# Kernel optimization log

Measured on AMD Instinct MI355X. Metric: run time of the kernel, lower is better.

The kernel has to match this reference:

```python
import jax, jax.numpy as jnp
import numpy as np

B, S, D = 2, 2048, 1024
H, DQK, DV = 16, 64, 64

def setup_inputs() -> dict:
    key = jax.random.key(0)
    k1, k2, k3, k4, k5 = jax.random.split(key, 5)
    scale_in = 1.0 / np.sqrt(D)
    scale_v = 1.0 / np.sqrt(H * DV)
    return {
        "x":   jax.random.normal(k1, (B, S, D), dtype=jnp.float32),
        "W_q": jax.random.uniform(k2, (D, H * DQK), minval=-scale_in, maxval=scale_in, dtype=jnp.float32),
        "W_k": jax.random.uniform(k3, (D, H * DQK), minval=-scale_in, maxval=scale_in, dtype=jnp.float32),
        "W_v": jax.random.uniform(k4, (D, H * DV), minval=-scale_in, maxval=scale_in, dtype=jnp.float32),
        "W_o": jax.random.uniform(k5, (H * DV, D), minval=-scale_v, maxval=scale_v, dtype=jnp.float32),
    }

def reference(x, W_q, W_k, W_v, W_o):
    b, s, _ = x.shape
    # projections -> [B, H, S, d]
    Q = (x @ W_q).reshape(b, s, H, DQK).transpose(0, 2, 1, 3)
    K = (x @ W_k).reshape(b, s, H, DQK).transpose(0, 2, 1, 3)
    V = (x @ W_v).reshape(b, s, H, DV).transpose(0, 2, 1, 3)
    scores = jnp.einsum('bhqd,bhkd->bhqk', Q, K) / np.sqrt(DQK).astype(np.float32)
    causal_mask = jnp.triu(jnp.ones((s, s), dtype=bool), k=1)  # True above diagonal
    scores = jnp.where(causal_mask[None, None], -jnp.inf, scores)
    attn = jax.nn.softmax(scores, axis=-1)
    out = jnp.einsum('bhqk,bhkd->bhqd', attn, V)  # [B,H,S,DV]
    out = out.transpose(0, 2, 1, 3).reshape(b, s, H * DV)
    return out @ W_o
```

## Files before the change

kernel.cpp:

```cpp
#include <hip/hip_runtime.h>


typedef float  f32x4  __attribute__((ext_vector_type(4)));
typedef __bf16 bf16x8 __attribute__((ext_vector_type(8)));

__device__ __forceinline__ unsigned short f2bf(float f) {
    __bf16 h = (__bf16)f;
    return __builtin_bit_cast(unsigned short, h);
}

__device__ __forceinline__ void gld16(unsigned short* lds, const unsigned short* g) {
    __builtin_amdgcn_global_load_lds(
        (const __attribute__((address_space(1))) void*)g,
        (__attribute__((address_space(3))) void*)lds, 16, 0, 0);
}

__global__ __launch_bounds__(256) void prep(const float* __restrict__ x,
                                            const float* __restrict__ W0,
                                            const float* __restrict__ W1,
                                            const float* __restrict__ W2,
                                            const float* __restrict__ W3,
                                            unsigned short* __restrict__ xb,
                                            unsigned short* __restrict__ WT) {
    __shared__ float T[64][65];
    const int blk = blockIdx.x;
    const int tid = threadIdx.x;
    if (blk < 4096) {
        size_t i = ((size_t)blk * 256 + tid) * 4;
        float4 v = *(const float4*)(x + i);
        ushort4 o;
        o.x = f2bf(v.x); o.y = f2bf(v.y); o.z = f2bf(v.z); o.w = f2bf(v.w);
        *(ushort4*)(xb + i) = o;
        return;
    }
    const int t = blk - 4096;
    const int z = t >> 8;
    const int k0 = ((t >> 4) & 15) * 64, n0 = (t & 15) * 64;
    const float* W = (z == 0) ? W0 : (z == 1) ? W1 : (z == 2) ? W2 : W3;
#pragma unroll
    for (int i = 0; i < 4; i++) {
        int c = tid + i * 256;
        int r = c >> 4, col = (c & 15) * 4;
        float4 v = *(const float4*)(W + (size_t)(k0 + r) * 1024 + n0 + col);
        T[r][col] = v.x; T[r][col + 1] = v.y; T[r][col + 2] = v.z; T[r][col + 3] = v.w;
    }
    __syncthreads();
    unsigned short* out = WT + (size_t)z * 1024 * 1024;
#pragma unroll
    for (int i = 0; i < 2; i++) {
        int c = tid + i * 256;
        int nr = c >> 3, koff = (c & 7) * 8;
        union { unsigned short us[8]; uint4 v; } pk;
#pragma unroll
        for (int j = 0; j < 8; j++) pk.us[j] = f2bf(T[koff + j][nr]);
        *(uint4*)(out + (size_t)(n0 + nr) * 1024 + k0 + koff) = pk.v;
    }
}

__global__ __launch_bounds__(256) void gemm_qkv(const unsigned short* __restrict__ A,
                                                const unsigned short* __restrict__ WTall,
                                                unsigned short* __restrict__ outq,
                                                unsigned short* __restrict__ Vp) {
    __shared__ unsigned short As0[128 * 64];
    __shared__ unsigned short Bs0[128 * 64];
    __shared__ unsigned short As1[128 * 64];
    __shared__ unsigned short Bs1[128 * 64];
    const int tid = threadIdx.x;
    const int w = tid >> 6, lane = tid & 63, quad = lane >> 4, ln = lane & 15;

    const int blk = blockIdx.x;
    const int n0 = ((blk >> 3) & 7) * 128;
    const int g  = ((blk >> 6) << 3) | (blk & 7);
    const int z  = g >> 5;
    const int m0 = (g & 31) * 128;

    const unsigned short* BT = WTall + (size_t)z * (1024 * 1024);
    const float scl = (z == 0) ? 0.180336878f : 1.0f;
    const bool swp = (z < 2);

    const int lr8 = lane >> 3;
    const int lc8 = ((lane & 7) ^ lr8) * 8;
    const int fsw = (quad ^ (ln & 7)) * 8;

    const f32x4 z4 = {0.f, 0.f, 0.f, 0.f};
    f32x4 acc[4][4];
#pragma unroll
    for (int i = 0; i < 4; i++)
#pragma unroll
        for (int j = 0; j < 4; j++) acc[i][j] = z4;

    const int wm = (w & 1) * 64, wn = (w >> 1) * 64;
    const int Rb = w * 32;

#define QKV_STAGE(Ad, Bd, kk)                                                              \
    {                                                                                      \
        _Pragma("unroll")                                                                  \
        for (int s = 0; s < 4; s++) {                                                      \
            gld16(Ad + (Rb + s * 8) * 64, A  + (size_t)(m0 + Rb + s * 8 + lr8) * 1024 + (kk) + lc8); \
            gld16(Bd + (Rb + s * 8) * 64, BT + (size_t)(n0 + Rb + s * 8 + lr8) * 1024 + (kk) + lc8); \
        }                                                                                  \
    }

#define QKV_COMPUTE(Ad, Bd)                                                                \
    {                                                                                      \
        _Pragma("unroll")                                                                  \
        for (int ks = 0; ks < 2; ks++) {                                                   \
            const int co = fsw ^ (ks * 32);                                                \
            bf16x8 af[4], bfr[4];                                                          \
            _Pragma("unroll")                                                              \
            for (int t = 0; t < 4; t++)                                                    \
                af[t] = *(const bf16x8*)&Ad[(wm + t * 16 + ln) * 64 + co];                 \
            _Pragma("unroll")                                                              \
            for (int t = 0; t < 4; t++)                                                    \
                bfr[t] = *(const bf16x8*)&Bd[(wn + t * 16 + ln) * 64 + co];                \
            if (swp) {                                                                     \
                _Pragma("unroll")                                                          \
                for (int tm = 0; tm < 4; tm++)                                             \
                    _Pragma("unroll")                                                      \
                    for (int tn = 0; tn < 4; tn++)                                         \
                        acc[tm][tn] = __builtin_amdgcn_mfma_f32_16x16x32_bf16(             \
                            bfr[tn], af[tm], acc[tm][tn], 0, 0, 0);                        \
            } else {                                                                       \
                _Pragma("unroll")                                                          \
                for (int tm = 0; tm < 4; tm++)                                             \
                    _Pragma("unroll")                                                      \
                    for (int tn = 0; tn < 4; tn++)                                         \
                        acc[tm][tn] = __builtin_amdgcn_mfma_f32_16x16x32_bf16(             \
                            af[tm], bfr[tn], acc[tm][tn], 0, 0, 0);                        \
            }                                                                              \
        }                                                                                  \
    }

    QKV_STAGE(As0, Bs0, 0);
    for (int k0 = 0; k0 < 1024; k0 += 128) {
        __syncthreads();
        if (k0 + 64 < 1024) QKV_STAGE(As1, Bs1, k0 + 64);
        QKV_COMPUTE(As0, Bs0);
        __syncthreads();
        if (k0 + 128 < 1024) QKV_STAGE(As0, Bs0, k0 + 128);
        if (k0 + 64 < 1024) QKV_COMPUTE(As1, Bs1);
    }
#undef QKV_STAGE
#undef QKV_COMPUTE

    if (swp) {
#pragma unroll
        for (int tm = 0; tm < 4; tm++)
#pragma unroll
            for (int tn = 0; tn < 4; tn++) {
                int mg = m0 + wm + tm * 16 + ln;
                int nb = n0 + wn + tn * 16 + quad * 4;
                int b = mg >> 11, s = mg & 2047, h = nb >> 6, dd = nb & 63;
                ushort4 o;
                o.x = f2bf(acc[tm][tn][0] * scl);
                o.y = f2bf(acc[tm][tn][1] * scl);
                o.z = f2bf(acc[tm][tn][2] * scl);
                o.w = f2bf(acc[tm][tn][3] * scl);
                size_t zoff = (size_t)z * (4096 * 1024);
                *(ushort4*)(outq + zoff + (((size_t)(b * 16 + h) * 2048 + s) << 6) + dd) = o;
            }
    } else {
#pragma unroll
        for (int tm = 0; tm < 4; tm++)
#pragma unroll
            for (int tn = 0; tn < 4; tn++) {
                int mg = m0 + wm + tm * 16 + quad * 4;
                int ng = n0 + wn + tn * 16 + ln;
                int b = mg >> 11, h = ng >> 6, dd = ng & 63;
                int sblk = (mg & 2047) & ~63;
                int cb = tm >> 1, t16 = tm & 1;
                int pp = cb * 32 + quad * 8 + t16 * 4;
                ushort4 o;
                o.x = f2bf(acc[tm][tn][0]);
                o.y = f2bf(acc[tm][tn][1]);
                o.z = f2bf(acc[tm][tn][2]);
                o.w = f2bf(acc[tm][tn][3]);
                *(ushort4*)(Vp + ((size_t)(b * 16 + h) * 64 + dd) * 2048 + sblk + pp) = o;
            }
    }
}

__global__ __launch_bounds__(256) void gemm_o(const unsigned short* __restrict__ A,
                                              const unsigned short* __restrict__ BT,
                                              float* __restrict__ outf) {
    __shared__ unsigned short As0[128 * 64];
    __shared__ unsigned short Bs0[128 * 64];
    __shared__ unsigned short As1[128 * 64];
    __shared__ unsigned short Bs1[128 * 64];
    const int tid = threadIdx.x;
    const int w = tid >> 6, lane = tid & 63, quad = lane >> 4, ln = lane & 15;

    const int blk = blockIdx.x;
    const int n0 = ((blk >> 3) & 7) * 128;
    const int m0 = (((blk >> 6) << 3) | (blk & 7)) * 128;

    const int lr8 = lane >> 3;
    const int lc8 = ((lane & 7) ^ lr8) * 8;
    const int fsw = (quad ^ (ln & 7)) * 8;

    const f32x4 z4 = {0.f, 0.f, 0.f, 0.f};
    f32x4 acc[4][4];
#pragma unroll
    for (int i = 0; i < 4; i++)
#pragma unroll
        for (int j = 0; j < 4; j++) acc[i][j] = z4;

    const int wm = (w & 1) * 64, wn = (w >> 1) * 64;
    const int Rb = w * 32;

#define O_STAGE(Ad, Bd, kk)                                                                \
    {                                                                                      \
        _Pragma("unroll")                                                                  \
        for (int s = 0; s < 4; s++) {                                                      \
            gld16(Ad + (Rb + s * 8) * 64, A  + (size_t)(m0 + Rb + s * 8 + lr8) * 1024 + (kk) + lc8); \
            gld16(Bd + (Rb + s * 8) * 64, BT + (size_t)(n0 + Rb + s * 8 + lr8) * 1024 + (kk) + lc8); \
        }                                                                                  \
    }

#define O_COMPUTE(Ad, Bd)                                                                  \
    {                                                                                      \
        _Pragma("unroll")                                                                  \
        for (int ks = 0; ks < 2; ks++) {                                                   \
            const int co = fsw ^ (ks * 32);                                                \
            bf16x8 af[4], bfr[4];                                                          \
            _Pragma("unroll")                                                              \
            for (int t = 0; t < 4; t++)                                                    \
                af[t] = *(const bf16x8*)&Ad[(wm + t * 16 + ln) * 64 + co];                 \
            _Pragma("unroll")                                                              \
            for (int t = 0; t < 4; t++)                                                    \
                bfr[t] = *(const bf16x8*)&Bd[(wn + t * 16 + ln) * 64 + co];                \
            _Pragma("unroll")                                                              \
            for (int tm = 0; tm < 4; tm++)                                                 \
                _Pragma("unroll")                                                          \
                for (int tn = 0; tn < 4; tn++)                                             \
                    acc[tm][tn] = __builtin_amdgcn_mfma_f32_16x16x32_bf16(                 \
                        bfr[tn], af[tm], acc[tm][tn], 0, 0, 0);                            \
        }                                                                                  \
    }

    O_STAGE(As0, Bs0, 0);
    for (int k0 = 0; k0 < 1024; k0 += 128) {
        __syncthreads();
        if (k0 + 64 < 1024) O_STAGE(As1, Bs1, k0 + 64);
        O_COMPUTE(As0, Bs0);
        __syncthreads();
        if (k0 + 128 < 1024) O_STAGE(As0, Bs0, k0 + 128);
        if (k0 + 64 < 1024) O_COMPUTE(As1, Bs1);
    }
#undef O_STAGE
#undef O_COMPUTE

#pragma unroll
    for (int tm = 0; tm < 4; tm++)
#pragma unroll
        for (int tn = 0; tn < 4; tn++) {
            int mg = m0 + wm + tm * 16 + ln;
            int nb = n0 + wn + tn * 16 + quad * 4;
            *(f32x4*)(outf + (size_t)mg * 1024 + nb) = acc[tm][tn];
        }
}

__global__ __launch_bounds__(512, 4) void flash(const unsigned short* __restrict__ Qb,
                                                const unsigned short* __restrict__ Kb,
                                                const unsigned short* __restrict__ Vpb,
                                                unsigned short* __restrict__ AO,
                                                float* __restrict__ Ph0,
                                                float* __restrict__ Ph1,
                                                float* __restrict__ Lb) {
    __shared__ __align__(16) unsigned short Ks[2][64 * 64];
    __shared__ __align__(16) unsigned short Vs[2][64 * 64];
    const int tid = threadIdx.x, w = tid >> 6, lane = tid & 63;
    const int qd = lane >> 4, ln = lane & 15;
    const int lr = lane >> 3;
    const int lchunk = (lane & 7) ^ lr;
    const int psw = (qd ^ (ln & 7)) * 8;

    const int blk = blockIdx.x;
    const int bh = blk & 31;
    const int s  = blk >> 5;
    int qi, kstart, kend, half;
    bool heavy;
    if (s < 8) {
        qi = s; kstart = 0; kend = (qi + 1) * 128; half = 0; heavy = false;
    } else {
        int t = s - 8; half = t >> 3; qi = 15 - (t & 7); heavy = true;
        int mid = (qi + 1) * 64;
        kstart = half ? mid : 0;
        kend   = half ? (qi + 1) * 128 : mid;
    }
    const int qt0 = qi * 128;

    const unsigned short* Kg = Kb  + (size_t)bh * 2048 * 64;
    const unsigned short* Vg = Vpb + (size_t)bh * 64 * 2048;

    bf16x8 aq[2];
    {
        const unsigned short* Qrow = Qb + ((size_t)bh * 2048 + qt0 + w * 16 + ln) * 64 + qd * 8;
        aq[0] = *(const bf16x8*)(Qrow);
        aq[1] = *(const bf16x8*)(Qrow + 32);
    }

    const f32x4 z4 = {0.f, 0.f, 0.f, 0.f};
    f32x4 Oc[4];
#pragma unroll
    for (int td = 0; td < 4; td++) Oc[td] = z4;
    float lsum = 0.f;

    const int qrow = qt0 + w * 16 + ln;
    const int qmin = qt0 + w * 16;
    const int qmax = qmin + 15;

#define FLASH_STAGE(buf, kk)                                                          \
    {                                                                                 \
        const unsigned short* kg = Kg + (size_t)((kk) + w * 8 + lr) * 64 + lchunk * 8; \
        gld16(&Ks[buf][(w * 8) * 64], kg);                                            \
        const unsigned short* vg = Vg + (size_t)(w * 8 + lr) * 2048 + (kk) + lchunk * 8; \
        gld16(&Vs[buf][(w * 8) * 64], vg);                                            \
    }

    FLASH_STAGE(0, kstart);
    int cur = 0;

    for (int k0 = kstart; k0 < kend; k0 += 64) {
        __syncthreads();
        if (k0 + 64 < kend) FLASH_STAGE(cur ^ 1, k0 + 64);

        if (k0 <= qmax) {
            f32x4 sc[4];
#pragma unroll
            for (int t = 0; t < 4; t++) {
                sc[t] = z4;
                if (k0 + t * 16 <= qmax) {
                    int off = (t * 16 + ln) * 64 + psw;
                    bf16x8 bk0 = *(const bf16x8*)&Ks[cur][off];
                    bf16x8 bk1 = *(const bf16x8*)&Ks[cur][off ^ 32];
                    sc[t] = __builtin_amdgcn_mfma_f32_16x16x32_bf16(bk0, aq[0], sc[t], 0, 0, 0);
                    sc[t] = __builtin_amdgcn_mfma_f32_16x16x32_bf16(bk1, aq[1], sc[t], 0, 0, 0);
                }
            }

            unsigned int pk[4][2];
#pragma unroll
            for (int t = 0; t < 4; t++) {
                if (k0 + t * 16 > qmax) { pk[t][0] = 0u; pk[t][1] = 0u; continue; }
                float e[4];
#pragma unroll
                for (int r2 = 0; r2 < 4; r2++) e[r2] = __builtin_amdgcn_exp2f(sc[t][r2]);
                if (k0 + t * 16 + 15 > qmin) {
#pragma unroll
                    for (int r2 = 0; r2 < 4; r2++)
                        if (k0 + t * 16 + qd * 4 + r2 > qrow) e[r2] = 0.f;
                }
                lsum += (e[0] + e[1]) + (e[2] + e[3]);
                pk[t][0] = (unsigned int)f2bf(e[0]) | ((unsigned int)f2bf(e[1]) << 16);
                pk[t][1] = (unsigned int)f2bf(e[2]) | ((unsigned int)f2bf(e[3]) << 16);
            }

            union { unsigned int u[4]; bf16x8 v; } apu0, apu1;
            apu0.u[0] = pk[0][0]; apu0.u[1] = pk[0][1]; apu0.u[2] = pk[1][0]; apu0.u[3] = pk[1][1];
            apu1.u[0] = pk[2][0]; apu1.u[1] = pk[2][1]; apu1.u[2] = pk[3][0]; apu1.u[3] = pk[3][1];
#pragma unroll
            for (int td = 0; td < 4; td++) {
                int voff = (td * 16 + ln) * 64 + psw;
                bf16x8 av0 = *(const bf16x8*)&Vs[cur][voff];
                bf16x8 av1 = *(const bf16x8*)&Vs[cur][voff ^ 32];
                Oc[td] = __builtin_amdgcn_mfma_f32_16x16x32_bf16(av0, apu0.v, Oc[td], 0, 0, 0);
                Oc[td] = __builtin_amdgcn_mfma_f32_16x16x32_bf16(av1, apu1.v, Oc[td], 0, 0, 0);
            }
        }
        cur ^= 1;
    }
#undef FLASH_STAGE

    lsum += __shfl_xor(lsum, 16);
    lsum += __shfl_xor(lsum, 32);

    if (!heavy) {
        const float inv = 1.0f / lsum;
        const int bz = bh >> 4, h = bh & 15;
        const int rowg = qt0 + w * 16 + ln;
        unsigned short* aorow = AO + ((size_t)(bz * 2048 + rowg) << 10) + h * 64 + qd * 4;
#pragma unroll
        for (int td = 0; td < 4; td++) {
            ushort4 o;
            o.x = f2bf(Oc[td][0] * inv);
            o.y = f2bf(Oc[td][1] * inv);
            o.z = f2bf(Oc[td][2] * inv);
            o.w = f2bf(Oc[td][3] * inv);
            *(ushort4*)(aorow + td * 16) = o;
        }
    } else {
        float* P = half ? Ph1 : Ph0;
        const int prow = ((bh * 8 + (qi - 8)) * 128) + w * 16 + ln;
        float* Pr = P + (size_t)prow * 64 + qd * 4;
#pragma unroll
        for (int td = 0; td < 4; td++)
            *(f32x4*)(Pr + td * 16) = Oc[td];
        if (qd == 0) Lb[half * 32768 + prow] = lsum;
    }
}

__global__ __launch_bounds__(256) void merge(const float* __restrict__ P0,
                                             const float* __restrict__ P1,
                                             const float* __restrict__ Lb,
                                             unsigned short* __restrict__ AO) {
    const int idx = blockIdx.x * 256 + threadIdx.x;
    const int d0 = (idx & 7) * 8;
    const int row = idx >> 3;
    const float inv = 1.0f / (Lb[row] + Lb[32768 + row]);
    const float* a = P0 + (size_t)row * 64 + d0;
    const float* b = P1 + (size_t)row * 64 + d0;
    f32x4 x0 = *(const f32x4*)a, x1 = *(const f32x4*)(a + 4);
    f32x4 y0 = *(const f32x4*)b, y1 = *(const f32x4*)(b + 4);
    union { unsigned short us[8]; uint4 v; } pk;
#pragma unroll
    for (int j = 0; j < 4; j++) {
        pk.us[j]     = f2bf((x0[j] + y0[j]) * inv);
        pk.us[j + 4] = f2bf((x1[j] + y1[j]) * inv);
    }
    const int bh = row >> 10, qi8 = (row >> 7) & 7, q = row & 127;
    const int bz = bh >> 4, h = bh & 15;
    const int rowg = (qi8 + 8) * 128 + q;
    *(uint4*)(AO + ((size_t)(bz * 2048 + rowg) << 10) + h * 64 + d0) = pk.v;
}

extern "C" void kernel_launch(void* const* d_in, const int* in_sizes, int n_in,
                              void* d_out, int out_size, void* d_ws, size_t ws_size,
                              hipStream_t stream) {
    const float* x  = (const float*)d_in[0];
    const float* Wq = (const float*)d_in[1];
    const float* Wk = (const float*)d_in[2];
    const float* Wv = (const float*)d_in[3];
    const float* Wo = (const float*)d_in[4];
    float* out = (float*)d_out;

    unsigned short* xb  = (unsigned short*)d_ws;
    unsigned short* WT  = xb  + (size_t)4096 * 1024;
    unsigned short* Qb  = WT  + (size_t)4 * 1024 * 1024;
    unsigned short* Kb  = Qb  + (size_t)4096 * 1024;
    unsigned short* Vb  = Kb  + (size_t)4096 * 1024;
    unsigned short* Vpb = Vb  + (size_t)4096 * 1024;
    unsigned short* AO  = Vpb + (size_t)4096 * 1024;

    float* Ph0 = (float*)Vb;
    float* Ph1 = (float*)xb;
    float* Lb  = (float*)WT;

    prep<<<dim3(5120), 256, 0, stream>>>(x, Wq, Wk, Wv, Wo, xb, WT);
    gemm_qkv<<<dim3(768), 256, 0, stream>>>(xb, WT, Qb, Vpb);
    flash<<<dim3(768), 512, 0, stream>>>(Qb, Kb, Vpb, AO, Ph0, Ph1, Lb);
    merge<<<dim3(1024), 256, 0, stream>>>(Ph0, Ph1, Lb, AO);
    gemm_o<<<dim3(256), 256, 0, stream>>>(AO, WT + (size_t)3 * 1024 * 1024, out);
}
```

Measured before the change: 170.0 us.

## Triple-buffer K/V tiles in flash kernel with partial vmcnt waits

Replaces the double-buffered K/V LDS staging in the flash attention kernel with a three-stage ring, unrolled by three. It waits with s_waitcnt vmcnt(2) so the next tile's loads can stay in flight across the barrier. The aim is to hide global-to-LDS load latency behind the MFMA work. LDS per block grows from 32KB to 48KB, which may lower occupancy at 512 threads with launch bounds of 4.

```diff
diff --git a/kernel.cpp b/kernel.cpp
--- a/kernel.cpp
+++ b/kernel.cpp
@@ -267,8 +267,12 @@
                                                 float* __restrict__ Ph0,
                                                 float* __restrict__ Ph1,
                                                 float* __restrict__ Lb) {
-    __shared__ __align__(16) unsigned short Ks[2][64 * 64];
-    __shared__ __align__(16) unsigned short Vs[2][64 * 64];
+    __shared__ __align__(16) unsigned short Ks0[64 * 64];
+    __shared__ __align__(16) unsigned short Vs0[64 * 64];
+    __shared__ __align__(16) unsigned short Ks1[64 * 64];
+    __shared__ __align__(16) unsigned short Vs1[64 * 64];
+    __shared__ __align__(16) unsigned short Ks2[64 * 64];
+    __shared__ __align__(16) unsigned short Vs2[64 * 64];
     const int tid = threadIdx.x, w = tid >> 6, lane = tid & 63;
     const int qd = lane >> 4, ln = lane & 15;
     const int lr = lane >> 3;
@@ -310,67 +314,86 @@
     const int qmin = qt0 + w * 16;
     const int qmax = qmin + 15;
 
-#define FLASH_STAGE(buf, kk)                                                          \
-    {                                                                                 \
-        const unsigned short* kg = Kg + (size_t)((kk) + w * 8 + lr) * 64 + lchunk * 8; \
-        gld16(&Ks[buf][(w * 8) * 64], kg);                                            \
+#define FLASH_STAGE(KD, VD, kk)                                                          \
+    {                                                                                    \
+        const unsigned short* kg = Kg + (size_t)((kk) + w * 8 + lr) * 64 + lchunk * 8;   \
+        gld16(&KD[(w * 8) * 64], kg);                                                    \
         const unsigned short* vg = Vg + (size_t)(w * 8 + lr) * 2048 + (kk) + lchunk * 8; \
-        gld16(&Vs[buf][(w * 8) * 64], vg);                                            \
-    }
-
-    FLASH_STAGE(0, kstart);
-    int cur = 0;
-
-    for (int k0 = kstart; k0 < kend; k0 += 64) {
-        __syncthreads();
-        if (k0 + 64 < kend) FLASH_STAGE(cur ^ 1, k0 + 64);
-
-        if (k0 <= qmax) {
-            f32x4 sc[4];
-#pragma unroll
-            for (int t = 0; t < 4; t++) {
-                sc[t] = z4;
-                if (k0 + t * 16 <= qmax) {
-                    int off = (t * 16 + ln) * 64 + psw;
-                    bf16x8 bk0 = *(const bf16x8*)&Ks[cur][off];
-                    bf16x8 bk1 = *(const bf16x8*)&Ks[cur][off ^ 32];
-                    sc[t] = __builtin_amdgcn_mfma_f32_16x16x32_bf16(bk0, aq[0], sc[t], 0, 0, 0);
-                    sc[t] = __builtin_amdgcn_mfma_f32_16x16x32_bf16(bk1, aq[1], sc[t], 0, 0, 0);
-                }
-            }
-
-            unsigned int pk[4][2];
-#pragma unroll
-            for (int t = 0; t < 4; t++) {
-                if (k0 + t * 16 > qmax) { pk[t][0] = 0u; pk[t][1] = 0u; continue; }
-                float e[4];
-#pragma unroll
-                for (int r2 = 0; r2 < 4; r2++) e[r2] = __builtin_amdgcn_exp2f(sc[t][r2]);
-                if (k0 + t * 16 + 15 > qmin) {
-#pragma unroll
-                    for (int r2 = 0; r2 < 4; r2++)
-                        if (k0 + t * 16 + qd * 4 + r2 > qrow) e[r2] = 0.f;
-                }
-                lsum += (e[0] + e[1]) + (e[2] + e[3]);
-                pk[t][0] = (unsigned int)f2bf(e[0]) | ((unsigned int)f2bf(e[1]) << 16);
-                pk[t][1] = (unsigned int)f2bf(e[2]) | ((unsigned int)f2bf(e[3]) << 16);
-            }
-
-            union { unsigned int u[4]; bf16x8 v; } apu0, apu1;
-            apu0.u[0] = pk[0][0]; apu0.u[1] = pk[0][1]; apu0.u[2] = pk[1][0]; apu0.u[3] = pk[1][1];
-            apu1.u[0] = pk[2][0]; apu1.u[1] = pk[2][1]; apu1.u[2] = pk[3][0]; apu1.u[3] = pk[3][1];
-#pragma unroll
-            for (int td = 0; td < 4; td++) {
-                int voff = (td * 16 + ln) * 64 + psw;
-                bf16x8 av0 = *(const bf16x8*)&Vs[cur][voff];
-                bf16x8 av1 = *(const bf16x8*)&Vs[cur][voff ^ 32];
-                Oc[td] = __builtin_amdgcn_mfma_f32_16x16x32_bf16(av0, apu0.v, Oc[td], 0, 0, 0);
-                Oc[td] = __builtin_amdgcn_mfma_f32_16x16x32_bf16(av1, apu1.v, Oc[td], 0, 0, 0);
-            }
+        gld16(&VD[(w * 8) * 64], vg);                                                    \
+    }
+
+#define FLASH_SYNC(more)                                                                 \
+    {                                                                                    \
+        if (more) { asm volatile("s_waitcnt vmcnt(2)" ::: "memory"); }                   \
+        else      { asm volatile("s_waitcnt vmcnt(0)" ::: "memory"); }                   \
+        __builtin_amdgcn_s_barrier();                                                    \
+        __builtin_amdgcn_sched_barrier(0);                                               \
+    }
+
+#define FLASH_TILE(KD, VD, kk)                                                           \
+    if ((kk) <= qmax) {                                                                  \
+        f32x4 sc[4];                                                                     \
+        _Pragma("unroll")                                                                \
+        for (int t = 0; t < 4; t++) {                                                    \
+            sc[t] = z4;                                                                  \
+            if ((kk) + t * 16 <= qmax) {                                                 \
+                int off = (t * 16 + ln) * 64 + psw;                                      \
+                bf16x8 bk0 = *(const bf16x8*)&KD[off];                                   \
+                bf16x8 bk1 = *(const bf16x8*)&KD[off ^ 32];                              \
+                sc[t] = __builtin_amdgcn_mfma_f32_16x16x32_bf16(bk0, aq[0], sc[t], 0, 0, 0); \
+                sc[t] = __builtin_amdgcn_mfma_f32_16x16x32_bf16(bk1, aq[1], sc[t], 0, 0, 0); \
+            }                                                                            \
+        }                                                                                \
+        unsigned int pk[4][2];                                                           \
+        _Pragma("unroll")                                                                \
+        for (int t = 0; t < 4; t++) {                                                    \
+            if ((kk) + t * 16 > qmax) { pk[t][0] = 0u; pk[t][1] = 0u; continue; }        \
+            float e[4];                                                                  \
+            _Pragma("unroll")                                                            \
+            for (int r2 = 0; r2 < 4; r2++) e[r2] = __builtin_amdgcn_exp2f(sc[t][r2]);    \
+            if ((kk) + t * 16 + 15 > qmin) {                                             \
+                _Pragma("unroll")                                                        \
+                for (int r2 = 0; r2 < 4; r2++)                                           \
+                    if ((kk) + t * 16 + qd * 4 + r2 > qrow) e[r2] = 0.f;                 \
+            }                                                                            \
+            lsum += (e[0] + e[1]) + (e[2] + e[3]);                                       \
+            pk[t][0] = (unsigned int)f2bf(e[0]) | ((unsigned int)f2bf(e[1]) << 16);      \
+            pk[t][1] = (unsigned int)f2bf(e[2]) | ((unsigned int)f2bf(e[3]) << 16);      \
+        }                                                                                \
+        union { unsigned int u[4]; bf16x8 v; } apu0, apu1;                               \
+        apu0.u[0] = pk[0][0]; apu0.u[1] = pk[0][1]; apu0.u[2] = pk[1][0]; apu0.u[3] = pk[1][1]; \
+        apu1.u[0] = pk[2][0]; apu1.u[1] = pk[2][1]; apu1.u[2] = pk[3][0]; apu1.u[3] = pk[3][1]; \
+        _Pragma("unroll")                                                                \
+        for (int td = 0; td < 4; td++) {                                                 \
+            int voff = (td * 16 + ln) * 64 + psw;                                        \
+            bf16x8 av0 = *(const bf16x8*)&VD[voff];                                      \
+            bf16x8 av1 = *(const bf16x8*)&VD[voff ^ 32];                                 \
+            Oc[td] = __builtin_amdgcn_mfma_f32_16x16x32_bf16(av0, apu0.v, Oc[td], 0, 0, 0); \
+            Oc[td] = __builtin_amdgcn_mfma_f32_16x16x32_bf16(av1, apu1.v, Oc[td], 0, 0, 0); \
+        }                                                                                \
+    }
+
+    FLASH_STAGE(Ks0, Vs0, kstart);
+    if (kstart + 64 < kend) FLASH_STAGE(Ks1, Vs1, kstart + 64);
+
+    for (int k0 = kstart; k0 < kend; k0 += 192) {
+        FLASH_SYNC(k0 + 64 < kend);
+        if (k0 + 128 < kend) FLASH_STAGE(Ks2, Vs2, k0 + 128);
+        FLASH_TILE(Ks0, Vs0, k0);
+        if (k0 + 64 < kend) {
+            FLASH_SYNC(k0 + 128 < kend);
+            if (k0 + 192 < kend) FLASH_STAGE(Ks0, Vs0, k0 + 192);
+            FLASH_TILE(Ks1, Vs1, k0 + 64);
         }
-        cur ^= 1;
+        if (k0 + 128 < kend) {
+            FLASH_SYNC(k0 + 192 < kend);
+            if (k0 + 256 < kend) FLASH_STAGE(Ks1, Vs1, k0 + 256);
+            FLASH_TILE(Ks2, Vs2, k0 + 128);
+        }
     }
 #undef FLASH_STAGE
+#undef FLASH_SYNC
+#undef FLASH_TILE
 
     lsum += __shfl_xor(lsum, 16);
     lsum += __shfl_xor(lsum, 32);
```

New measurement: 166.8 us, median of 3. No clear change (-1.9%).
